# Kernel tuning notes

Hardware: AMD Instinct MI355X
Metric: run time of the kernel (lower is better)

The kernel has to match this reference:

```python
import jax, jax.numpy as jnp
import numpy as np

B, T, F = 64, 1000, 512
H, KD = 8, 32
EPS = 1e-6


def setup_inputs() -> dict:
    key = jax.random.key(0)
    ks = jax.random.split(key, 12)
    s_in = 1.0 / np.sqrt(F)
    s_out = 1.0 / np.sqrt(H * KD)
    return {
        "x": jax.random.normal(ks[0], (B, T, F), jnp.float32),
        "q": jax.random.normal(ks[1], (F,), jnp.float32) * s_in,      # global_query (1,1,F) squeezed
        "Wq": jax.random.normal(ks[2], (F, H, KD), jnp.float32) * s_in,
        "bq": jnp.zeros((H, KD), jnp.float32),
        "Wk": jax.random.normal(ks[3], (F, H, KD), jnp.float32) * s_in,
        "bk": jnp.zeros((H, KD), jnp.float32),
        "Wv": jax.random.normal(ks[4], (F, H, KD), jnp.float32) * s_in,
        "bv": jnp.zeros((H, KD), jnp.float32),
        "Wo": jax.random.normal(ks[5], (H, KD, F), jnp.float32) * s_out,
        "bo": jnp.zeros((F,), jnp.float32),
        "Wd": jax.random.normal(ks[6], (F, F), jnp.float32) * s_in,    # Dense, use_bias=False
        "gamma": jnp.ones((F,), jnp.float32),
        "beta": jnp.zeros((F,), jnp.float32),
    }


def reference(x, q, Wq, bq, Wk, bk, Wv, bv, Wo, bo, Wd, gamma, beta):
    # Single learned query attends over full sequence (keras MultiHeadAttention semantics).
    qh = jnp.einsum('f,fhk->hk', q, Wq) + bq                   # (H, KD), shared across batch
    kh = jnp.einsum('btf,fhk->bthk', x, Wk) + bk               # (B, T, H, KD)
    vh = jnp.einsum('btf,fhk->bthk', x, Wv) + bv               # (B, T, H, KD)
    scale = 1.0 / jnp.sqrt(jnp.asarray(KD, x.dtype))
    scores = jnp.einsum('hk,bthk->bht', qh, kh) * scale        # (B, H, T)
    attn = jax.nn.softmax(scores, axis=-1)
    ctx = jnp.einsum('bht,bthk->bhk', attn, vh)                # (B, H, KD)
    pooled = jnp.einsum('bhk,hkf->bf', ctx, Wo) + bo           # (B, F) attention output proj
    out = pooled @ Wd                                          # Dense, no bias
    mu = jnp.mean(out, axis=-1, keepdims=True)
    var = jnp.mean(jnp.square(out - mu), axis=-1, keepdims=True)
    return (out - mu) * jax.lax.rsqrt(var + EPS) * gamma + beta
```

## Files before the change

kernel.cpp:

```cpp
#include <hip/hip_runtime.h>
#include <cstddef>

#define B_ 64
#define T_ 1000
#define F_ 512
#define H_ 8
#define KD_ 32
#define HK_ 256
#define NC_ 8
#define CT_ 125

__global__ __launch_bounds__(64) void k_qh(const float* __restrict__ q,
                                           const float* __restrict__ Wq,
                                           const float* __restrict__ bq,
                                           float* __restrict__ qh) {
    int hk = blockIdx.x;
    int lane = threadIdx.x;
    float s = 0.f;
    for (int f = lane; f < F_; f += 64) s += q[f] * Wq[(size_t)f * HK_ + hk];
    #pragma unroll
    for (int off = 32; off; off >>= 1) s += __shfl_down(s, off);
    if (lane == 0) qh[hk] = s + bq[hk];
}

__global__ __launch_bounds__(256) void k_wk(const float* __restrict__ qh,
                                            const float* __restrict__ Wk,
                                            const float* __restrict__ bk,
                                            float* __restrict__ wk,
                                            float* __restrict__ ck) {
    int f = blockIdx.x;
    int tid = threadIdx.x;
    __shared__ float red[256];
    red[tid] = qh[tid] * Wk[(size_t)f * HK_ + tid];
    __syncthreads();
    #pragma unroll
    for (int off = 16; off; off >>= 1) {
        if ((tid & 31) < off) red[tid] += red[tid + off];
        __syncthreads();
    }
    if ((tid & 31) == 0) wk[f * H_ + (tid >> 5)] = red[tid];
    if (f == 0 && tid < H_) {
        float c = 0.f;
        for (int k = 0; k < KD_; k++) c += qh[tid * KD_ + k] * bk[tid * KD_ + k];
        ck[tid] = c;
    }
}

__global__ __launch_bounds__(512) void k_weff(const float* __restrict__ Wo,
                                              const float* __restrict__ Wd,
                                              const float* __restrict__ bo,
                                              float* __restrict__ weff,
                                              float* __restrict__ bwd) {
    int sub = blockIdx.x % 257;
    int gi = blockIdx.x / 257;
    int f = threadIdx.x;
    int g0 = gi * 128;
    if (sub < HK_) {
        const float* wo = Wo + (size_t)sub * F_ + g0;
        float s = 0.f;
        #pragma unroll 8
        for (int g = 0; g < 128; g++) s += wo[g] * Wd[(size_t)(g0 + g) * F_ + f];
        atomicAdd(&weff[(size_t)sub * F_ + f], s);
    } else {
        float s = 0.f;
        #pragma unroll 8
        for (int g = 0; g < 128; g++) s += bo[g0 + g] * Wd[(size_t)(g0 + g) * F_ + f];
        atomicAdd(&bwd[f], s);
    }
}

__global__ __launch_bounds__(128) void k_fused(const float* __restrict__ x,
                                               const float* __restrict__ wk,
                                               const float* __restrict__ ck,
                                               float* __restrict__ part,
                                               float2* __restrict__ ml2) {
    __shared__ __align__(16) float at[CT_ + 3][H_];
    const int c = blockIdx.x & (NC_ - 1);
    const int b = blockIdx.x >> 3;
    const int tid = threadIdx.x;
    const float scale = 0.17677669529663687f;

    if (tid < CT_) {
        const float4* xr = (const float4*)(x + ((size_t)b * T_ + (size_t)c * CT_ + tid) * F_);
        float acc[H_] = {0.f,0.f,0.f,0.f,0.f,0.f,0.f,0.f};
        for (int ii = 0; ii < 16; ii++) {
            float4 xv[8];
            #pragma unroll
            for (int u = 0; u < 8; u++) xv[u] = xr[ii * 8 + u];
            #pragma unroll
            for (int u = 0; u < 8; u++) {
                const float* wr = wk + (size_t)(ii * 8 + u) * 32;
                #pragma unroll
                for (int h = 0; h < H_; h++)
                    acc[h] += xv[u].x * wr[h]      + xv[u].y * wr[8 + h]
                            + xv[u].z * wr[16 + h] + xv[u].w * wr[24 + h];
            }
        }
        #pragma unroll
        for (int h = 0; h < H_; h++) at[tid][h] = (acc[h] + ck[h]) * scale;
    }
    __syncthreads();

    {
        const int h = tid >> 4, j = tid & 15;
        float m = -3.0e38f;
        for (int t = j; t < CT_; t += 16) m = fmaxf(m, at[t][h]);
        #pragma unroll
        for (int off = 8; off; off >>= 1) m = fmaxf(m, __shfl_xor(m, off, 16));
        float l = 0.f;
        for (int t = j; t < CT_; t += 16) {
            float p = __expf(at[t][h] - m);
            at[t][h] = p;
            l += p;
        }
        #pragma unroll
        for (int off = 8; off; off >>= 1) l += __shfl_xor(l, off, 16);
        if (j == 0) ml2[(size_t)(c * B_ + b) * H_ + h] = make_float2(m, l);
    }
    __syncthreads();

    {
        const float4* xc = (const float4*)(x + ((size_t)b * T_ + (size_t)c * CT_) * F_) + tid;
        float4 a[H_];
        #pragma unroll
        for (int h = 0; h < H_; h++) a[h] = make_float4(0.f, 0.f, 0.f, 0.f);
        #pragma unroll 5
        for (int t = 0; t < CT_; t++) {
            const float4 xv = xc[(size_t)t * 128];
            #pragma unroll
            for (int h = 0; h < H_; h++) {
                const float p = at[t][h];
                a[h].x += p * xv.x; a[h].y += p * xv.y;
                a[h].z += p * xv.z; a[h].w += p * xv.w;
            }
        }
        float4* dst = (float4*)(part + (size_t)(c * B_ + b) * (H_ * F_));
        #pragma unroll
        for (int h = 0; h < H_; h++) dst[h * 128 + tid] = a[h];
    }
}

__global__ __launch_bounds__(512) void k_tail(const float* __restrict__ part,
                                              const float2* __restrict__ ml2,
                                              const float* __restrict__ Wv,
                                              const float* __restrict__ bv,
                                              const float* __restrict__ weff,
                                              const float* __restrict__ bwd,
                                              const float* __restrict__ gamma,
                                              const float* __restrict__ beta,
                                              float* __restrict__ out) {
    int b = blockIdx.x;
    int tid = threadIdx.x;
    __shared__ float coef[NC_][H_];
    __shared__ float xs[H_ * F_];
    __shared__ float ctx_s[HK_];
    __shared__ float red[512];
    __shared__ float stat[2];

    if (tid < H_) {
        int h = tid;
        float M = -3.0e38f;
        #pragma unroll
        for (int c = 0; c < NC_; c++)
            M = fmaxf(M, ml2[(size_t)(c * B_ + b) * H_ + h].x);
        float L = 0.f;
        #pragma unroll
        for (int c = 0; c < NC_; c++) {
            float2 d = ml2[(size_t)(c * B_ + b) * H_ + h];
            L += __expf(d.x - M) * d.y;
        }
        float invL = 1.0f / L;
        #pragma unroll
        for (int c = 0; c < NC_; c++) {
            float2 d = ml2[(size_t)(c * B_ + b) * H_ + h];
            coef[c][h] = __expf(d.x - M) * invL;
        }
    }
    __syncthreads();

    for (int i = tid; i < H_ * F_; i += 512) {
        int h = i >> 9;
        float s = 0.f;
        #pragma unroll
        for (int c = 0; c < NC_; c++)
            s += coef[c][h] * part[(size_t)(c * B_ + b) * (H_ * F_) + i];
        xs[i] = s;
    }
    __syncthreads();

    {
        int hk = tid & 255;
        int half = tid >> 8;
        int h = hk >> 5;
        int fb = half * 256;
        float s = 0.f;
        #pragma unroll 8
        for (int j = 0; j < 256; j++) {
            int f = fb + j;
            s += xs[h * F_ + f] * Wv[(size_t)f * HK_ + hk];
        }
        red[tid] = s;
        __syncthreads();
        if (tid < 256) ctx_s[tid] = red[tid] + red[tid + 256] + bv[tid];
    }
    __syncthreads();

    float o = bwd[tid];
    #pragma unroll 8
    for (int hk = 0; hk < HK_; hk++) o += ctx_s[hk] * weff[(size_t)hk * F_ + tid];

    {
        float v1 = o, v2 = o * o;
        #pragma unroll
        for (int off = 32; off; off >>= 1) {
            v1 += __shfl_down(v1, off);
            v2 += __shfl_down(v2, off);
        }
        int lane = tid & 63, wid = tid >> 6;
        if (lane == 0) { red[wid] = v1; red[8 + wid] = v2; }
        __syncthreads();
        if (tid == 0) {
            float s1 = 0.f, s2 = 0.f;
            #pragma unroll
            for (int ww = 0; ww < 8; ww++) { s1 += red[ww]; s2 += red[8 + ww]; }
            float mu = s1 * (1.0f / F_);
            float var = s2 * (1.0f / F_) - mu * mu;
            stat[0] = mu;
            stat[1] = rsqrtf(var + 1e-6f);
        }
        __syncthreads();
    }
    float mu = stat[0], rstd = stat[1];
    out[(size_t)b * F_ + tid] = (o - mu) * rstd * gamma[tid] + beta[tid];
}

extern "C" void kernel_launch(void* const* d_in, const int* in_sizes, int n_in,
                              void* d_out, int out_size, void* d_ws, size_t ws_size,
                              hipStream_t stream) {
    const float* x     = (const float*)d_in[0];
    const float* q     = (const float*)d_in[1];
    const float* Wq    = (const float*)d_in[2];
    const float* bq    = (const float*)d_in[3];
    const float* Wk    = (const float*)d_in[4];
    const float* bk    = (const float*)d_in[5];
    const float* Wv    = (const float*)d_in[6];
    const float* bv    = (const float*)d_in[7];
    const float* Wo    = (const float*)d_in[8];
    const float* bo    = (const float*)d_in[9];
    const float* Wd    = (const float*)d_in[10];
    const float* gamma = (const float*)d_in[11];
    const float* beta  = (const float*)d_in[12];
    float* out = (float*)d_out;

    char* ws = (char*)d_ws;
    float*  qh   = (float*)(ws + 0);
    float*  wk   = (float*)(ws + 4096);
    float*  ck   = (float*)(ws + 20480);
    float*  weff = (float*)(ws + 24576);
    float*  bwd  = (float*)(ws + 548864);
    float2* ml2  = (float2*)(ws + 557056);
    float*  part = (float*)(ws + 589824);

    hipMemsetAsync(ws + 24576, 0, 526336, stream);
    k_qh<<<HK_, 64, 0, stream>>>(q, Wq, bq, qh);
    k_wk<<<F_, 256, 0, stream>>>(qh, Wk, bk, wk, ck);
    k_weff<<<4 * 257, 512, 0, stream>>>(Wo, Wd, bo, weff, bwd);
    k_fused<<<B_ * NC_, 128, 0, stream>>>(x, wk, ck, part, ml2);
    k_tail<<<B_, 512, 0, stream>>>(part, ml2, Wv, bv, weff, bwd, gamma, beta, out);
}
```

Baseline: 295.2 us.

## Widen fused attention blocks, split tail into ctx and output kernels

The main attention kernel now runs 512 threads per block. The score computation is split into four feature quarters that are reduced through shared memory, softmax runs one wave per head, and the weighted sum uses scalar per-thread columns. The precomputed Wo·Wd product kernel is removed, and the output projections are applied directly in a new kernel that handles two batch rows per block. The tail is split into a context kernel spread over four feature quarters with atomic accumulation, plus that output kernel. The aim is more parallelism in the dominant pass over x and less serialized work per tail block. The cost is extra shared-memory reductions and an additional kernel launch.

```diff
diff --git a/kernel.cpp b/kernel.cpp
--- a/kernel.cpp
+++ b/kernel.cpp
@@ -46,50 +46,33 @@
     }
 }
 
-__global__ __launch_bounds__(512) void k_weff(const float* __restrict__ Wo,
-                                              const float* __restrict__ Wd,
-                                              const float* __restrict__ bo,
-                                              float* __restrict__ weff,
-                                              float* __restrict__ bwd) {
-    int sub = blockIdx.x % 257;
-    int gi = blockIdx.x / 257;
-    int f = threadIdx.x;
-    int g0 = gi * 128;
-    if (sub < HK_) {
-        const float* wo = Wo + (size_t)sub * F_ + g0;
-        float s = 0.f;
-        #pragma unroll 8
-        for (int g = 0; g < 128; g++) s += wo[g] * Wd[(size_t)(g0 + g) * F_ + f];
-        atomicAdd(&weff[(size_t)sub * F_ + f], s);
-    } else {
-        float s = 0.f;
-        #pragma unroll 8
-        for (int g = 0; g < 128; g++) s += bo[g0 + g] * Wd[(size_t)(g0 + g) * F_ + f];
-        atomicAdd(&bwd[f], s);
-    }
-}
-
-__global__ __launch_bounds__(128) void k_fused(const float* __restrict__ x,
+__global__ __launch_bounds__(512) void k_fused(const float* __restrict__ x,
                                                const float* __restrict__ wk,
                                                const float* __restrict__ ck,
                                                float* __restrict__ part,
                                                float2* __restrict__ ml2) {
-    __shared__ __align__(16) float at[CT_ + 3][H_];
+    __shared__ float atp[128][4][H_ + 1];
+    __shared__ float at[128][H_];
     const int c = blockIdx.x & (NC_ - 1);
     const int b = blockIdx.x >> 3;
     const int tid = threadIdx.x;
+    const int lane = tid & 63;
+    const int w = __builtin_amdgcn_readfirstlane(tid >> 6);
+    const int qw = w & 3, rh = w >> 2;
+    const int row = rh * 64 + lane;
     const float scale = 0.17677669529663687f;
 
-    if (tid < CT_) {
-        const float4* xr = (const float4*)(x + ((size_t)b * T_ + (size_t)c * CT_ + tid) * F_);
+    if (row < CT_) {
         float acc[H_] = {0.f,0.f,0.f,0.f,0.f,0.f,0.f,0.f};
-        for (int ii = 0; ii < 16; ii++) {
+        const float4* xr = (const float4*)(x + ((size_t)b * T_ + (size_t)c * CT_ + row) * F_) + qw * 32;
+        const float* wkq = wk + qw * 128 * H_;
+        for (int ii = 0; ii < 4; ii++) {
             float4 xv[8];
             #pragma unroll
             for (int u = 0; u < 8; u++) xv[u] = xr[ii * 8 + u];
             #pragma unroll
             for (int u = 0; u < 8; u++) {
-                const float* wr = wk + (size_t)(ii * 8 + u) * 32;
+                const float* wr = wkq + (ii * 8 + u) * 32;
                 #pragma unroll
                 for (int h = 0; h < H_; h++)
                     acc[h] += xv[u].x * wr[h]      + xv[u].y * wr[8 + h]
@@ -97,141 +80,161 @@
             }
         }
         #pragma unroll
-        for (int h = 0; h < H_; h++) at[tid][h] = (acc[h] + ck[h]) * scale;
-    }
-    __syncthreads();
-
-    {
-        const int h = tid >> 4, j = tid & 15;
-        float m = -3.0e38f;
-        for (int t = j; t < CT_; t += 16) m = fmaxf(m, at[t][h]);
-        #pragma unroll
-        for (int off = 8; off; off >>= 1) m = fmaxf(m, __shfl_xor(m, off, 16));
-        float l = 0.f;
-        for (int t = j; t < CT_; t += 16) {
-            float p = __expf(at[t][h] - m);
-            at[t][h] = p;
-            l += p;
-        }
-        #pragma unroll
-        for (int off = 8; off; off >>= 1) l += __shfl_xor(l, off, 16);
-        if (j == 0) ml2[(size_t)(c * B_ + b) * H_ + h] = make_float2(m, l);
-    }
-    __syncthreads();
-
-    {
-        const float4* xc = (const float4*)(x + ((size_t)b * T_ + (size_t)c * CT_) * F_) + tid;
-        float4 a[H_];
-        #pragma unroll
-        for (int h = 0; h < H_; h++) a[h] = make_float4(0.f, 0.f, 0.f, 0.f);
-        #pragma unroll 5
+        for (int h = 0; h < H_; h++) atp[row][qw][h] = acc[h];
+    }
+    __syncthreads();
+
+    for (int i = tid; i < CT_ * H_; i += 512) {
+        int r = i >> 3, h = i & 7;
+        at[r][h] = (atp[r][0][h] + atp[r][1][h] + atp[r][2][h] + atp[r][3][h] + ck[h]) * scale;
+    }
+    __syncthreads();
+
+    {
+        const int h = w;
+        const int t1 = lane + 64;
+        float s0 = (lane < CT_) ? at[lane][h] : -3.0e38f;
+        float s1 = (t1 < CT_) ? at[t1][h] : -3.0e38f;
+        float m = fmaxf(s0, s1);
+        #pragma unroll
+        for (int off = 32; off; off >>= 1) m = fmaxf(m, __shfl_xor(m, off));
+        float p0 = (lane < CT_) ? __expf(s0 - m) : 0.f;
+        float p1 = (t1 < CT_) ? __expf(s1 - m) : 0.f;
+        if (lane < CT_) at[lane][h] = p0;
+        if (t1 < CT_) at[t1][h] = p1;
+        float l = p0 + p1;
+        #pragma unroll
+        for (int off = 32; off; off >>= 1) l += __shfl_xor(l, off);
+        if (lane == 0) ml2[(size_t)(c * B_ + b) * H_ + h] = make_float2(m, l);
+    }
+    __syncthreads();
+
+    {
+        const float* xc = x + ((size_t)b * T_ + (size_t)c * CT_) * F_ + tid;
+        float a[H_] = {0.f,0.f,0.f,0.f,0.f,0.f,0.f,0.f};
+        #pragma unroll 8
         for (int t = 0; t < CT_; t++) {
-            const float4 xv = xc[(size_t)t * 128];
-            #pragma unroll
-            for (int h = 0; h < H_; h++) {
-                const float p = at[t][h];
-                a[h].x += p * xv.x; a[h].y += p * xv.y;
-                a[h].z += p * xv.z; a[h].w += p * xv.w;
-            }
-        }
-        float4* dst = (float4*)(part + (size_t)(c * B_ + b) * (H_ * F_));
-        #pragma unroll
-        for (int h = 0; h < H_; h++) dst[h * 128 + tid] = a[h];
-    }
-}
-
-__global__ __launch_bounds__(512) void k_tail(const float* __restrict__ part,
-                                              const float2* __restrict__ ml2,
-                                              const float* __restrict__ Wv,
-                                              const float* __restrict__ bv,
-                                              const float* __restrict__ weff,
-                                              const float* __restrict__ bwd,
-                                              const float* __restrict__ gamma,
-                                              const float* __restrict__ beta,
-                                              float* __restrict__ out) {
-    int b = blockIdx.x;
-    int tid = threadIdx.x;
-    __shared__ float coef[NC_][H_];
-    __shared__ float xs[H_ * F_];
-    __shared__ float ctx_s[HK_];
-    __shared__ float red[512];
-    __shared__ float stat[2];
-
-    if (tid < H_) {
-        int h = tid;
-        float M = -3.0e38f;
+            const float xv = xc[(size_t)t * F_];
+            #pragma unroll
+            for (int h = 0; h < H_; h++) a[h] += at[t][h] * xv;
+        }
+        float* dst = part + (size_t)(c * B_ + b) * (H_ * F_) + tid;
+        #pragma unroll
+        for (int h = 0; h < H_; h++) dst[h * F_] = a[h];
+    }
+}
+
+__global__ __launch_bounds__(256) void k_ctx(const float* __restrict__ part,
+                                             const float2* __restrict__ ml2,
+                                             const float* __restrict__ Wv,
+                                             float* __restrict__ ctx) {
+    __shared__ float coefL[NC_][H_];
+    __shared__ float xsq[H_][132];
+    const int b = blockIdx.x >> 2;
+    const int fq = blockIdx.x & 3;
+    const int tid = threadIdx.x;
+
+    if (tid < 64) {
+        const int c = tid >> 3, h = tid & 7;
+        const float2 d = ml2[(size_t)(c * B_ + b) * H_ + h];
+        float M = d.x;
+        #pragma unroll
+        for (int off = 8; off < 64; off <<= 1) M = fmaxf(M, __shfl_xor(M, off));
+        const float e = __expf(d.x - M);
+        float Lt = e * d.y;
+        #pragma unroll
+        for (int off = 8; off < 64; off <<= 1) Lt += __shfl_xor(Lt, off);
+        coefL[c][h] = e / Lt;
+    }
+    __syncthreads();
+
+    for (int i = tid; i < H_ * 128; i += 256) {
+        const int h = i >> 7, fl = i & 127;
+        float s = 0.f;
         #pragma unroll
         for (int c = 0; c < NC_; c++)
-            M = fmaxf(M, ml2[(size_t)(c * B_ + b) * H_ + h].x);
-        float L = 0.f;
-        #pragma unroll
-        for (int c = 0; c < NC_; c++) {
-            float2 d = ml2[(size_t)(c * B_ + b) * H_ + h];
-            L += __expf(d.x - M) * d.y;
-        }
-        float invL = 1.0f / L;
-        #pragma unroll
-        for (int c = 0; c < NC_; c++) {
-            float2 d = ml2[(size_t)(c * B_ + b) * H_ + h];
-            coef[c][h] = __expf(d.x - M) * invL;
-        }
-    }
-    __syncthreads();
-
-    for (int i = tid; i < H_ * F_; i += 512) {
-        int h = i >> 9;
-        float s = 0.f;
-        #pragma unroll
-        for (int c = 0; c < NC_; c++)
-            s += coef[c][h] * part[(size_t)(c * B_ + b) * (H_ * F_) + i];
-        xs[i] = s;
-    }
-    __syncthreads();
-
-    {
-        int hk = tid & 255;
-        int half = tid >> 8;
-        int h = hk >> 5;
-        int fb = half * 256;
-        float s = 0.f;
-        #pragma unroll 8
-        for (int j = 0; j < 256; j++) {
-            int f = fb + j;
-            s += xs[h * F_ + f] * Wv[(size_t)f * HK_ + hk];
-        }
-        red[tid] = s;
-        __syncthreads();
-        if (tid < 256) ctx_s[tid] = red[tid] + red[tid + 256] + bv[tid];
-    }
-    __syncthreads();
-
-    float o = bwd[tid];
+            s += coefL[c][h] * part[(size_t)(c * B_ + b) * (H_ * F_) + h * F_ + fq * 128 + fl];
+        xsq[h][fl] = s;
+    }
+    __syncthreads();
+
+    const int hk = tid, h = hk >> 5;
+    float s = 0.f;
     #pragma unroll 8
-    for (int hk = 0; hk < HK_; hk++) o += ctx_s[hk] * weff[(size_t)hk * F_ + tid];
-
-    {
-        float v1 = o, v2 = o * o;
+    for (int j = 0; j < 128; j++)
+        s += xsq[h][j] * Wv[(size_t)(fq * 128 + j) * HK_ + hk];
+    atomicAdd(&ctx[(size_t)b * HK_ + hk], s);
+}
+
+__global__ __launch_bounds__(512) void k_out(const float* __restrict__ ctx,
+                                             const float* __restrict__ bv,
+                                             const float* __restrict__ Wo,
+                                             const float* __restrict__ bo,
+                                             const float* __restrict__ Wd,
+                                             const float* __restrict__ gamma,
+                                             const float* __restrict__ beta,
+                                             float* __restrict__ out) {
+    __shared__ float ctxL[2][HK_];
+    __shared__ float pooledL[2][F_];
+    __shared__ float red[32];
+    __shared__ float stat[4];
+    const int b0 = blockIdx.x * 2;
+    const int tid = threadIdx.x;
+
+    {
+        const int r = tid >> 8, hk = tid & 255;
+        ctxL[r][hk] = ctx[(size_t)(b0 + r) * HK_ + hk] + bv[hk];
+    }
+    __syncthreads();
+
+    float p0 = bo[tid], p1 = p0;
+    #pragma unroll 8
+    for (int hk = 0; hk < HK_; hk++) {
+        const float wo = Wo[(size_t)hk * F_ + tid];
+        p0 += ctxL[0][hk] * wo;
+        p1 += ctxL[1][hk] * wo;
+    }
+    pooledL[0][tid] = p0;
+    pooledL[1][tid] = p1;
+    __syncthreads();
+
+    float o0 = 0.f, o1 = 0.f;
+    #pragma unroll 8
+    for (int g = 0; g < F_; g++) {
+        const float wd = Wd[(size_t)g * F_ + tid];
+        o0 += pooledL[0][g] * wd;
+        o1 += pooledL[1][g] * wd;
+    }
+
+    {
+        float v1 = o0, v2 = o0 * o0, v3 = o1, v4 = o1 * o1;
         #pragma unroll
         for (int off = 32; off; off >>= 1) {
             v1 += __shfl_down(v1, off);
             v2 += __shfl_down(v2, off);
-        }
-        int lane = tid & 63, wid = tid >> 6;
-        if (lane == 0) { red[wid] = v1; red[8 + wid] = v2; }
+            v3 += __shfl_down(v3, off);
+            v4 += __shfl_down(v4, off);
+        }
+        const int lane = tid & 63, wid = tid >> 6;
+        if (lane == 0) { red[wid * 4] = v1; red[wid * 4 + 1] = v2; red[wid * 4 + 2] = v3; red[wid * 4 + 3] = v4; }
         __syncthreads();
         if (tid == 0) {
-            float s1 = 0.f, s2 = 0.f;
-            #pragma unroll
-            for (int ww = 0; ww < 8; ww++) { s1 += red[ww]; s2 += red[8 + ww]; }
-            float mu = s1 * (1.0f / F_);
-            float var = s2 * (1.0f / F_) - mu * mu;
-            stat[0] = mu;
-            stat[1] = rsqrtf(var + 1e-6f);
+            float s1 = 0.f, s2 = 0.f, s3 = 0.f, s4 = 0.f;
+            #pragma unroll
+            for (int ww = 0; ww < 8; ww++) {
+                s1 += red[ww * 4]; s2 += red[ww * 4 + 1]; s3 += red[ww * 4 + 2]; s4 += red[ww * 4 + 3];
+            }
+            const float mu0 = s1 * (1.0f / F_), mu1 = s3 * (1.0f / F_);
+            stat[0] = mu0;
+            stat[1] = rsqrtf(s2 * (1.0f / F_) - mu0 * mu0 + 1e-6f);
+            stat[2] = mu1;
+            stat[3] = rsqrtf(s4 * (1.0f / F_) - mu1 * mu1 + 1e-6f);
         }
         __syncthreads();
     }
-    float mu = stat[0], rstd = stat[1];
-    out[(size_t)b * F_ + tid] = (o - mu) * rstd * gamma[tid] + beta[tid];
+    const float g_ = gamma[tid], bt = beta[tid];
+    out[(size_t)b0 * F_ + tid]       = (o0 - stat[0]) * stat[1] * g_ + bt;
+    out[(size_t)(b0 + 1) * F_ + tid] = (o1 - stat[2]) * stat[3] * g_ + bt;
 }
 
 extern "C" void kernel_launch(void* const* d_in, const int* in_sizes, int n_in,
@@ -256,15 +259,14 @@
     float*  qh   = (float*)(ws + 0);
     float*  wk   = (float*)(ws + 4096);
     float*  ck   = (float*)(ws + 20480);
-    float*  weff = (float*)(ws + 24576);
-    float*  bwd  = (float*)(ws + 548864);
-    float2* ml2  = (float2*)(ws + 557056);
-    float*  part = (float*)(ws + 589824);
-
-    hipMemsetAsync(ws + 24576, 0, 526336, stream);
+    float2* ml2  = (float2*)(ws + 24576);
+    float*  ctx  = (float*)(ws + 65536);
+    float*  part = (float*)(ws + 1048576);
+
+    hipMemsetAsync(ctx, 0, B_ * HK_ * sizeof(float), stream);
     k_qh<<<HK_, 64, 0, stream>>>(q, Wq, bq, qh);
     k_wk<<<F_, 256, 0, stream>>>(qh, Wk, bk, wk, ck);
-    k_weff<<<4 * 257, 512, 0, stream>>>(Wo, Wd, bo, weff, bwd);
-    k_fused<<<B_ * NC_, 128, 0, stream>>>(x, wk, ck, part, ml2);
-    k_tail<<<B_, 512, 0, stream>>>(part, ml2, Wv, bv, weff, bwd, gamma, beta, out);
-}
+    k_fused<<<B_ * NC_, 512, 0, stream>>>(x, wk, ck, part, ml2);
+    k_ctx<<<B_ * 4, 256, 0, stream>>>(part, ml2, Wv, ctx);
+    k_out<<<B_ / 2, 512, 0, stream>>>(ctx, bv, Wo, bo, Wd, gamma, beta, out);
+}
```

Result: slower. 309.7 us (+4.9%).
